# Optimization experiments

Hardware: AMD Instinct MI355X
Metric: run time of the kernel (lower is better)

Reference implementation:

```python
import jax, jax.numpy as jnp
import numpy as np

N_JOINTS = 24

def _rodrigues(r):
    # r: [B, J, 3] axis-angle -> [B, J, 3, 3] rotation matrices
    theta = jnp.clip(jnp.linalg.norm(r, axis=-1, keepdims=True), 1e-6)  # [B,J,1]
    rh = r / theta
    z = jnp.zeros_like(rh[..., :1])
    # skew-symmetric matrix m
    m = jnp.stack([
        jnp.concatenate([z, -rh[..., 2:3], rh[..., 1:2]], -1),
        jnp.concatenate([rh[..., 2:3], z, -rh[..., 0:1]], -1),
        jnp.concatenate([-rh[..., 1:2], rh[..., 0:1], z], -1),
    ], axis=-2)  # [B,J,3,3]
    rrT = rh[..., :, None] * rh[..., None, :]  # outer product [B,J,3,3]
    cos = jnp.cos(theta)[..., None]
    sin = jnp.sin(theta)[..., None]
    eye = jnp.eye(3, dtype=r.dtype)
    return cos * eye + (1.0 - cos) * rrT + sin * m

def _with_zeros(Rm, t):
    # Rm: [B,3,3], t: [B,3] -> [B,4,4] homogeneous transform
    B = Rm.shape[0]
    top = jnp.concatenate([Rm, t[:, :, None]], axis=-1)  # [B,3,4]
    bot = jnp.broadcast_to(jnp.array([0.0, 0.0, 0.0, 1.0], Rm.dtype), (B, 1, 4))
    return jnp.concatenate([top, bot], axis=1)

def _keypoints(v, idx):
    # v: [B,N,3], idx: [G,K] vertex-index groups -> [B,G,3] via (max+min)/2
    g = v[:, idx]  # [B,G,K,3] irregular gather
    return (g.max(axis=2) + g.min(axis=2)) * 0.5

def setup_inputs() -> dict:
    key = jax.random.key(0)
    ks = jax.random.split(key, 8)
    B, N, P, K = 64, 40000, 100, 128
    beta = jax.random.normal(ks[0], (B, P), jnp.float32)
    pose = jax.random.normal(ks[1], (B, N_JOINTS * 3), jnp.float32) * 0.3
    trans = jax.random.normal(ks[2], (B, 3), jnp.float32)
    shapedirs = jax.random.normal(ks[3], (P, 3 * N), jnp.float32) * 0.01
    v_template = jax.random.normal(ks[4], (N, 3), jnp.float32)
    w = jax.random.uniform(ks[5], (N, N_JOINTS), jnp.float32)
    weights = w / w.sum(axis=1, keepdims=True)  # LBS weights sum to 1
    reorder_index = jnp.arange(N_JOINTS, dtype=jnp.int64 if jax.config.jax_enable_x64 else jnp.int32)
    # kinematic tree: parent[i] < i (binary-tree shape stands in for the rabbit skeleton)
    parent = jnp.concatenate([jnp.zeros(1, jnp.int32), (jnp.arange(1, N_JOINTS, dtype=jnp.int32) - 1) // 2])
    joint_idx = jax.random.randint(ks[6], (N_JOINTS - 1, K), 0, N)
    add_idx = jax.random.randint(ks[7], (7, K), 0, N)
    return {"beta": beta, "pose": pose, "trans": trans, "shapedirs": shapedirs,
            "v_template": v_template, "weights": weights, "reorder_index": reorder_index,
            "parent": parent, "joint_idx": joint_idx, "add_idx": add_idx}

def reference(beta, pose, trans, shapedirs, v_template, weights,
              reorder_index, parent, joint_idx, add_idx):
    B = beta.shape[0]
    pose = pose.reshape(B, N_JOINTS, 3)[:, reorder_index]
    # blend shapes: v_shaped = beta @ shapedirs + template
    v_posed = (beta @ shapedirs + v_template.reshape(-1)).reshape(B, -1, 3)  # [B,N,3]
    # joints from vertex-group (max+min)/2, root is zero
    J = jnp.concatenate([jnp.zeros((B, 1, 3), beta.dtype), _keypoints(v_posed, joint_idx)], axis=1)  # [B,24,3]
    R = _rodrigues(pose)  # [B,24,3,3]
    # forward kinematics along the tree (fixed 24-joint loop)
    par = np.asarray(jax.device_get(parent))
    G = [_with_zeros(R[:, 0], J[:, 0])]
    for i in range(1, N_JOINTS):
        p = int(par[i])
        G_loc = _with_zeros(R[:, i], J[:, i] - J[:, p])
        G.append(jnp.matmul(G[p], G_loc))
    G = jnp.stack(G, axis=1)  # [B,24,4,4]
    # remove rest-pose joint locations (pack subtraction only touches last column)
    Jh = jnp.concatenate([J, jnp.zeros((B, N_JOINTS, 1), beta.dtype)], axis=-1)[..., None]  # [B,24,4,1]
    t_corr = jnp.matmul(G, Jh)  # [B,24,4,1]
    G1 = jnp.concatenate([G[..., :3], G[..., 3:4] - t_corr], axis=-1)
    # LBS skinning: per-vertex blended transform
    T = jnp.einsum('nk,bkij->bnij', weights, G1)  # [B,N,4,4]
    vh = jnp.concatenate([v_posed, jnp.ones((B, v_posed.shape[1], 1), beta.dtype)], axis=-1)  # [B,N,4]
    posed = jnp.einsum('bnij,bnj->bni', T, vh)[..., :3] + trans[:, None, :]  # [B,N,3]
    skeleton = jnp.concatenate([
        jnp.zeros((B, 1, 3), beta.dtype),
        _keypoints(posed, joint_idx),
        _keypoints(posed, add_idx),
    ], axis=1)  # [B,31,3]
    return posed, skeleton
```

## Files before the change

kernel.cpp:

```cpp
#include <hip/hip_runtime.h>
#include <math.h>

#define B   64
#define NV  40000
#define P   100
#define KG  128
#define NJ  24
#define TVJ 16
#define TVS 32
#define NSK 31
#define NSUB (KG / TVJ)

typedef __attribute__((ext_vector_type(8))) short bf16x8;
typedef __attribute__((ext_vector_type(4))) float f32x4;

__device__ __forceinline__ unsigned short rne_bf16(float f) {
  unsigned u = __float_as_uint(f);
  u = (u + 0x7FFFu + ((u >> 16) & 1u)) >> 16;
  return (unsigned short)u;
}

__global__ __launch_bounds__(512)
void k_jpart(const float* __restrict__ beta,
             const float* __restrict__ sd,
             const float* __restrict__ vt,
             const int*   __restrict__ joint_idx,
             float*       __restrict__ pmn,
             float*       __restrict__ pmx) {
  const int j = blockIdx.x;
  const int s = blockIdx.y;
  const int t = threadIdx.x;
  const int lane = t & 63, wv = t >> 6;
  const int l15 = lane & 15, qd = lane >> 4;

  __shared__ __align__(16) unsigned short beta_s[64 * 136];
  __shared__ __align__(16) unsigned short sdT_s[48 * 136];
  __shared__ float vt_s[48];
  __shared__ int   idx_s[TVJ];
  float* pos_s = (float*)beta_s;

  if (t < TVJ) idx_s[t] = joint_idx[j * KG + s * TVJ + t];
  __syncthreads();

  for (int e = t; e < 64 * 36; e += 512) {
    const int m = e / 36, pp = P + e % 36;
    beta_s[m * 136 + pp] = 0;
  }
  for (int e = t; e < 64 * P; e += 512) {
    const int m = e / P, p = e % P;
    beta_s[m * 136 + p] = rne_bf16(beta[e]);
  }
  for (int task = t; task < 768; task += 512) {
    const int n = task % 48, kg = task / 48;
    const size_t colbase = (size_t)idx_s[n / 3] * 3 + (n % 3);
    unsigned pk[4];
#pragma unroll
    for (int h = 0; h < 4; ++h) {
      const int k0 = kg * 8 + 2 * h;
      float f0 = 0.0f, f1 = 0.0f;
      if (k0 < P)     f0 = sd[(size_t)k0 * (3 * NV) + colbase];
      if (k0 + 1 < P) f1 = sd[(size_t)(k0 + 1) * (3 * NV) + colbase];
      pk[h] = (unsigned)rne_bf16(f0) | ((unsigned)rne_bf16(f1) << 16);
    }
    *(uint4*)&sdT_s[n * 136 + kg * 8] = make_uint4(pk[0], pk[1], pk[2], pk[3]);
  }
  if (t < 48) vt_s[t] = vt[(size_t)idx_s[t / 3] * 3 + (t % 3)];
  __syncthreads();

  f32x4 acc[3];
  float vtv[3];
  if (wv < 4) {
    bf16x8 af[4];
#pragma unroll
    for (int ks = 0; ks < 4; ++ks)
      af[ks] = *(const bf16x8*)&beta_s[(wv * 16 + l15) * 136 + ks * 32 + qd * 8];
#pragma unroll
    for (int nt = 0; nt < 3; ++nt) acc[nt] = (f32x4){0.f, 0.f, 0.f, 0.f};
#pragma unroll
    for (int ks = 0; ks < 4; ++ks) {
#pragma unroll
      for (int nt = 0; nt < 3; ++nt) {
        const bf16x8 bf = *(const bf16x8*)&sdT_s[(nt * 16 + l15) * 136 + ks * 32 + qd * 8];
        acc[nt] = __builtin_amdgcn_mfma_f32_16x16x32_bf16(af[ks], bf, acc[nt], 0, 0, 0);
      }
    }
#pragma unroll
    for (int nt = 0; nt < 3; ++nt) vtv[nt] = vt_s[nt * 16 + l15];
  }
  __syncthreads();

  if (wv < 4) {
#pragma unroll
    for (int nt = 0; nt < 3; ++nt) {
      const int n = nt * 16 + l15;
      const int v = n / 3, c = n - 3 * v;
#pragma unroll
      for (int r = 0; r < 4; ++r) {
        const int m = wv * 16 + qd * 4 + r;
        pos_s[m * 68 + v * 4 + c] = acc[nt][r] + vtv[nt];
      }
    }
  }
  __syncthreads();

  if (t < 192) {
    const int b = t / 3, c = t % 3;
    float lo = 1e30f, hi = -1e30f;
#pragma unroll
    for (int v = 0; v < TVJ; ++v) {
      const float val = pos_s[b * 68 + v * 4 + c];
      lo = fminf(lo, val); hi = fmaxf(hi, val);
    }
    pmn[((j * NSUB + s) * B + b) * 3 + c] = lo;
    pmx[((j * NSUB + s) * B + b) * 3 + c] = hi;
  }
}

__global__ void k_chain(const float* __restrict__ pose,
                        const int*   __restrict__ parent,
                        const float* __restrict__ pmn,
                        const float* __restrict__ pmx,
                        const float* __restrict__ beta,
                        const float* __restrict__ trans,
                        unsigned short* __restrict__ G1A,
                        unsigned short* __restrict__ beta_bf) {
  const int b = blockIdx.x;
  const int t = threadIdx.x;

  __shared__ float R[NJ][9];
  __shared__ float Jl[NJ][3];
  __shared__ float G[NJ][12];
  __shared__ float G1c[NJ][12];

  if (t < NJ) {
    const float x = pose[b * NJ * 3 + t * 3 + 0];
    const float y = pose[b * NJ * 3 + t * 3 + 1];
    const float z = pose[b * NJ * 3 + t * 3 + 2];
    const float th = fmaxf(sqrtf(x * x + y * y + z * z), 1e-6f);
    const float xh = x / th, yh = y / th, zh = z / th;
    const float c = cosf(th), s = sinf(th), o = 1.0f - c;
    R[t][0] = c + o * xh * xh;      R[t][1] = o * xh * yh - s * zh; R[t][2] = o * xh * zh + s * yh;
    R[t][3] = o * xh * yh + s * zh; R[t][4] = c + o * yh * yh;      R[t][5] = o * yh * zh - s * xh;
    R[t][6] = o * xh * zh - s * yh; R[t][7] = o * yh * zh + s * xh; R[t][8] = c + o * zh * zh;
    if (t == 0) {
      Jl[0][0] = 0.0f; Jl[0][1] = 0.0f; Jl[0][2] = 0.0f;
    } else {
      const int jj = t - 1;
#pragma unroll
      for (int c2 = 0; c2 < 3; ++c2) {
        float lo = 1e30f, hi = -1e30f;
#pragma unroll
        for (int s2 = 0; s2 < NSUB; ++s2) {
          lo = fminf(lo, pmn[((jj * NSUB + s2) * B + b) * 3 + c2]);
          hi = fmaxf(hi, pmx[((jj * NSUB + s2) * B + b) * 3 + c2]);
        }
        Jl[t][c2] = 0.5f * (lo + hi);
      }
    }
  }
  __syncthreads();

  if (t < 12) {
    const int r = t >> 2, c = t & 3;
    G[0][t] = (c < 3) ? R[0][r * 3 + c] : Jl[0][r];
  }
  __syncthreads();

  for (int i = 1; i < NJ; ++i) {
    const int p = parent[i];
    if (t < 12) {
      const int r = t >> 2, c = t & 3;
      const float g0 = G[p][r * 4 + 0];
      const float g1 = G[p][r * 4 + 1];
      const float g2 = G[p][r * 4 + 2];
      float l0, l1, l2, add;
      if (c < 3) {
        l0 = R[i][0 * 3 + c]; l1 = R[i][1 * 3 + c]; l2 = R[i][2 * 3 + c];
        add = 0.0f;
      } else {
        l0 = Jl[i][0] - Jl[p][0]; l1 = Jl[i][1] - Jl[p][1]; l2 = Jl[i][2] - Jl[p][2];
        add = G[p][r * 4 + 3];
      }
      G[i][t] = g0 * l0 + g1 * l1 + g2 * l2 + add;
    }
    __syncthreads();
  }

  for (int e = t; e < NJ * 12; e += 64) {
    const int i = e / 12, rc = e % 12, r = rc >> 2, c = rc & 3;
    float val;
    if (c < 3) {
      val = G[i][rc];
    } else {
      val = G[i][r * 4 + 3] - (G[i][r * 4 + 0] * Jl[i][0] +
                               G[i][r * 4 + 1] * Jl[i][1] +
                               G[i][r * 4 + 2] * Jl[i][2]);
    }
    G1c[i][rc] = val;
  }
  __syncthreads();

  for (int e = t; e < 136; e += 64)
    beta_bf[b * 136 + e] = (e < P) ? rne_bf16(beta[b * P + e]) : (unsigned short)0;

  for (int e = t; e < 512; e += 64) {
    const int m = e >> 5, k = e & 31;
    float val = 0.0f;
    if (m < 12) {
      if (k < NJ) val = G1c[k][m];
      else if (k == NJ && (m & 3) == 3) val = trans[b * 3 + (m >> 2)];
    }
    G1A[(size_t)b * 512 + e] = rne_bf16(val);
  }
}

__global__ __launch_bounds__(256)
void k_skin(const float* __restrict__ sd,
            const float* __restrict__ vt,
            const float* __restrict__ w,
            const unsigned short* __restrict__ beta_bf,
            const unsigned short* __restrict__ G1A,
            float*       __restrict__ out) {
  const int n0v  = blockIdx.x * TVS;
  const int col0 = n0v * 3;
  const int t  = threadIdx.x;
  const int lane = t & 63, wv = t >> 6;
  const int l15 = lane & 15, q = lane >> 4;

  __shared__ __align__(16) unsigned char smem[46464];
  unsigned short* beta_s = (unsigned short*)smem;
  unsigned short* sdT_s  = (unsigned short*)(smem + 17408);
  unsigned short* wT_s   = (unsigned short*)(smem + 43520);
  float*          vt_s   = (float*)(smem + 46080);
  float*          vhf    = (float*)smem;

  for (int e = t; e < 1088; e += 256)
    ((uint4*)beta_s)[e] = ((const uint4*)beta_bf)[e];
  for (int task = t; task < 1536; task += 256) {
    const int n = task % 96, kg = task / 96;
    unsigned pk[4];
#pragma unroll
    for (int h = 0; h < 4; ++h) {
      const int k0 = kg * 8 + 2 * h;
      float f0 = 0.0f, f1 = 0.0f;
      if (k0 < P)     f0 = sd[(size_t)k0 * (3 * NV) + col0 + n];
      if (k0 + 1 < P) f1 = sd[(size_t)(k0 + 1) * (3 * NV) + col0 + n];
      pk[h] = (unsigned)rne_bf16(f0) | ((unsigned)rne_bf16(f1) << 16);
    }
    *(uint4*)&sdT_s[n * 136 + kg * 8] = make_uint4(pk[0], pk[1], pk[2], pk[3]);
  }
  for (int e = t; e < 1024; e += 256) {
    const int n = e >> 5, k = e & 31;
    float val = (k < NJ) ? w[(n0v + n) * NJ + k] : (k == NJ ? 1.0f : 0.0f);
    wT_s[n * 40 + k] = rne_bf16(val);
  }
  if (t < 96) vt_s[t] = vt[col0 + t];
  __syncthreads();

  bf16x8 af[4];
#pragma unroll
  for (int ks = 0; ks < 4; ++ks)
    af[ks] = *(const bf16x8*)&beta_s[(wv * 16 + l15) * 136 + ks * 32 + q * 8];
  f32x4 acc[6];
#pragma unroll
  for (int nt = 0; nt < 6; ++nt) acc[nt] = (f32x4){0.f, 0.f, 0.f, 0.f};
#pragma unroll
  for (int ks = 0; ks < 4; ++ks) {
#pragma unroll
    for (int nt = 0; nt < 6; ++nt) {
      const bf16x8 bf = *(const bf16x8*)&sdT_s[(nt * 16 + l15) * 136 + ks * 32 + q * 8];
      acc[nt] = __builtin_amdgcn_mfma_f32_16x16x32_bf16(af[ks], bf, acc[nt], 0, 0, 0);
    }
  }
  __syncthreads();

#pragma unroll
  for (int nt = 0; nt < 6; ++nt) {
    const int n = nt * 16 + l15;
    const int v = n / 3, c = n - 3 * v;
    const float vtn = vt_s[n];
#pragma unroll
    for (int r = 0; r < 4; ++r) {
      const int m = wv * 16 + q * 4 + r;
      vhf[m * 128 + v * 4 + c] = acc[nt][r] + vtn;
    }
  }
  __syncthreads();

  const bf16x8 wf0 = *(const bf16x8*)&wT_s[l15 * 40 + q * 8];
  const bf16x8 wf1 = *(const bf16x8*)&wT_s[(16 + l15) * 40 + q * 8];
  const f32x4 zero = (f32x4){0.f, 0.f, 0.f, 0.f};
#pragma unroll 4
  for (int bi = 0; bi < 16; ++bi) {
    const int b = wv * 16 + bi;
    const bf16x8 gf = *(const bf16x8*)&G1A[(size_t)b * 512 + l15 * 32 + q * 8];
    const f32x4 d0 = __builtin_amdgcn_mfma_f32_16x16x32_bf16(gf, wf0, zero, 0, 0, 0);
    const f32x4 d1 = __builtin_amdgcn_mfma_f32_16x16x32_bf16(gf, wf1, zero, 0, 0, 0);
    const float4 vh0 = *(const float4*)&vhf[b * 128 + l15 * 4];
    const float4 vh1 = *(const float4*)&vhf[b * 128 + 64 + l15 * 4];
    if (q < 3) {
      out[(size_t)b * (NV * 3) + col0 + l15 * 3 + q] =
          d0[0] * vh0.x + d0[1] * vh0.y + d0[2] * vh0.z + d0[3];
      out[(size_t)b * (NV * 3) + col0 + 48 + l15 * 3 + q] =
          d1[0] * vh1.x + d1[1] * vh1.y + d1[2] * vh1.z + d1[3];
    }
  }
}

__global__ void k_skel(const float* __restrict__ posed,
                       const int*   __restrict__ joint_idx,
                       const int*   __restrict__ add_idx,
                       float*       __restrict__ skel) {
  const int j = blockIdx.x;
  const int b = blockIdx.y;
  const int t = threadIdx.x;
  const int idx = (j < 23) ? joint_idx[j * KG + t] : add_idx[(j - 23) * KG + t];

  const float* p = posed + (size_t)b * NV * 3 + (size_t)idx * 3;
  float mn[3], mx[3];
#pragma unroll
  for (int c = 0; c < 3; ++c) { mn[c] = p[c]; mx[c] = p[c]; }
#pragma unroll
  for (int off = 32; off > 0; off >>= 1) {
#pragma unroll
    for (int c = 0; c < 3; ++c) {
      mn[c] = fminf(mn[c], __shfl_down(mn[c], off));
      mx[c] = fmaxf(mx[c], __shfl_down(mx[c], off));
    }
  }
  __shared__ float s_mn[2][3], s_mx[2][3];
  const int wave = t >> 6, lane = t & 63;
  if (lane == 0) {
#pragma unroll
    for (int c = 0; c < 3; ++c) { s_mn[wave][c] = mn[c]; s_mx[wave][c] = mx[c]; }
  }
  __syncthreads();
  if (t == 0) {
#pragma unroll
    for (int c = 0; c < 3; ++c) {
      float lo = fminf(s_mn[0][c], s_mn[1][c]);
      float hi = fmaxf(s_mx[0][c], s_mx[1][c]);
      skel[(b * NSK + 1 + j) * 3 + c] = 0.5f * (lo + hi);
      if (j == 0) skel[(b * NSK + 0) * 3 + c] = 0.0f;
    }
  }
}

extern "C" void kernel_launch(void* const* d_in, const int* in_sizes, int n_in,
                              void* d_out, int out_size, void* d_ws, size_t ws_size,
                              hipStream_t stream) {
  const float* beta     = (const float*)d_in[0];
  const float* pose     = (const float*)d_in[1];
  const float* trans    = (const float*)d_in[2];
  const float* sd       = (const float*)d_in[3];
  const float* vt       = (const float*)d_in[4];
  const float* w        = (const float*)d_in[5];
  const int* parent     = (const int*)d_in[7];
  const int* joint_idx  = (const int*)d_in[8];
  const int* add_idx    = (const int*)d_in[9];

  float* out = (float*)d_out;
  unsigned short* G1A     = (unsigned short*)d_ws;
  unsigned short* beta_bf = G1A + B * 512;
  float* pmn = (float*)(beta_bf + B * 136);
  float* pmx = pmn + 23 * NSUB * B * 3;

  k_jpart<<<dim3(23, NSUB), 512, 0, stream>>>(beta, sd, vt, joint_idx, pmn, pmx);
  k_chain<<<B, 64, 0, stream>>>(pose, parent, pmn, pmx, beta, trans, G1A, beta_bf);
  k_skin <<<NV / TVS, 256, 0, stream>>>(sd, vt, w, beta_bf, G1A, out);
  k_skel <<<dim3(30, B), 128, 0, stream>>>(out, joint_idx, add_idx,
                                           out + (size_t)B * NV * 3);
}
```

Before: 160.2 us.

## Fuse four kernels into two using atomic last-block and spin-wait tails

Merges the joint-partial kernel with the kinematic chain, so the last block to finish (found with an atomic counter) computes the forward kinematics for all 64 batches, one thread per batch. The skinning and skeleton kernels are also merged. The final 160 skinning blocks spin on a global counter until every block has written its output, then each does a share of the keypoint min/max reductions. This cuts launch count and inter-kernel gaps. The cost is a serial tail on one block, spin-waiting that depends on the waiting blocks being co-resident, and an extra memset launch.

```diff
diff --git a/kernel.cpp b/kernel.cpp
--- a/kernel.cpp
+++ b/kernel.cpp
@@ -1,15 +1,18 @@
 #include <hip/hip_runtime.h>
 #include <math.h>
 
-#define B   64
-#define NV  40000
-#define P   100
-#define KG  128
-#define NJ  24
-#define TVJ 16
-#define TVS 32
-#define NSK 31
+#define B    64
+#define NV   40000
+#define P    100
+#define KG   128
+#define NJ   24
+#define TVJ  16
+#define TVS  32
+#define NSK  31
 #define NSUB (KG / TVJ)
+#define NBLK (NV / TVS)
+#define NSPIN 160
+#define NTASK (30 * B)
 
 typedef __attribute__((ext_vector_type(8))) short bf16x8;
 typedef __attribute__((ext_vector_type(4))) float f32x4;
@@ -20,37 +23,44 @@
   return (unsigned short)u;
 }
 
-__global__ __launch_bounds__(512)
-void k_jpart(const float* __restrict__ beta,
-             const float* __restrict__ sd,
-             const float* __restrict__ vt,
-             const int*   __restrict__ joint_idx,
-             float*       __restrict__ pmn,
-             float*       __restrict__ pmx) {
+__global__ __launch_bounds__(256)
+void k_jc(const float* __restrict__ beta,
+          const float* __restrict__ sd,
+          const float* __restrict__ vt,
+          const int*   __restrict__ joint_idx,
+          const float* __restrict__ pose,
+          const float* __restrict__ trans,
+          float*       __restrict__ pmn,
+          float*       __restrict__ pmx,
+          unsigned short* __restrict__ G1A,
+          unsigned short* __restrict__ beta_bf,
+          int*         __restrict__ cnt) {
   const int j = blockIdx.x;
   const int s = blockIdx.y;
   const int t = threadIdx.x;
   const int lane = t & 63, wv = t >> 6;
   const int l15 = lane & 15, qd = lane >> 4;
 
-  __shared__ __align__(16) unsigned short beta_s[64 * 136];
-  __shared__ __align__(16) unsigned short sdT_s[48 * 136];
-  __shared__ float vt_s[48];
-  __shared__ int   idx_s[TVJ];
-  float* pos_s = (float*)beta_s;
+  __shared__ __align__(16) unsigned char smem[55296];
+  unsigned short* beta_s = (unsigned short*)smem;
+  unsigned short* sdT_s  = (unsigned short*)(smem + 17408);
+  float*          vt_s   = (float*)(smem + 30464);
+  int*            idx_s  = (int*)(smem + 30656);
+  float*          pos_s  = (float*)smem;
+  __shared__ int s_old;
 
   if (t < TVJ) idx_s[t] = joint_idx[j * KG + s * TVJ + t];
   __syncthreads();
 
-  for (int e = t; e < 64 * 36; e += 512) {
+  for (int e = t; e < 64 * 36; e += 256) {
     const int m = e / 36, pp = P + e % 36;
     beta_s[m * 136 + pp] = 0;
   }
-  for (int e = t; e < 64 * P; e += 512) {
+  for (int e = t; e < 64 * P; e += 256) {
     const int m = e / P, p = e % P;
     beta_s[m * 136 + p] = rne_bf16(beta[e]);
   }
-  for (int task = t; task < 768; task += 512) {
+  for (int task = t; task < 768; task += 256) {
     const int n = task % 48, kg = task / 48;
     const size_t colbase = (size_t)idx_s[n / 3] * 3 + (n % 3);
     unsigned pk[4];
@@ -67,38 +77,34 @@
   if (t < 48) vt_s[t] = vt[(size_t)idx_s[t / 3] * 3 + (t % 3)];
   __syncthreads();
 
+  bf16x8 af[4];
+#pragma unroll
+  for (int ks = 0; ks < 4; ++ks)
+    af[ks] = *(const bf16x8*)&beta_s[(wv * 16 + l15) * 136 + ks * 32 + qd * 8];
   f32x4 acc[3];
+#pragma unroll
+  for (int nt = 0; nt < 3; ++nt) acc[nt] = (f32x4){0.f, 0.f, 0.f, 0.f};
+#pragma unroll
+  for (int ks = 0; ks < 4; ++ks) {
+#pragma unroll
+    for (int nt = 0; nt < 3; ++nt) {
+      const bf16x8 bf = *(const bf16x8*)&sdT_s[(nt * 16 + l15) * 136 + ks * 32 + qd * 8];
+      acc[nt] = __builtin_amdgcn_mfma_f32_16x16x32_bf16(af[ks], bf, acc[nt], 0, 0, 0);
+    }
+  }
   float vtv[3];
-  if (wv < 4) {
-    bf16x8 af[4];
-#pragma unroll
-    for (int ks = 0; ks < 4; ++ks)
-      af[ks] = *(const bf16x8*)&beta_s[(wv * 16 + l15) * 136 + ks * 32 + qd * 8];
-#pragma unroll
-    for (int nt = 0; nt < 3; ++nt) acc[nt] = (f32x4){0.f, 0.f, 0.f, 0.f};
-#pragma unroll
-    for (int ks = 0; ks < 4; ++ks) {
-#pragma unroll
-      for (int nt = 0; nt < 3; ++nt) {
-        const bf16x8 bf = *(const bf16x8*)&sdT_s[(nt * 16 + l15) * 136 + ks * 32 + qd * 8];
-        acc[nt] = __builtin_amdgcn_mfma_f32_16x16x32_bf16(af[ks], bf, acc[nt], 0, 0, 0);
-      }
-    }
-#pragma unroll
-    for (int nt = 0; nt < 3; ++nt) vtv[nt] = vt_s[nt * 16 + l15];
-  }
-  __syncthreads();
-
-  if (wv < 4) {
-#pragma unroll
-    for (int nt = 0; nt < 3; ++nt) {
-      const int n = nt * 16 + l15;
-      const int v = n / 3, c = n - 3 * v;
-#pragma unroll
-      for (int r = 0; r < 4; ++r) {
-        const int m = wv * 16 + qd * 4 + r;
-        pos_s[m * 68 + v * 4 + c] = acc[nt][r] + vtv[nt];
-      }
+#pragma unroll
+  for (int nt = 0; nt < 3; ++nt) vtv[nt] = vt_s[nt * 16 + l15];
+  __syncthreads();
+
+#pragma unroll
+  for (int nt = 0; nt < 3; ++nt) {
+    const int n = nt * 16 + l15;
+    const int v = n / 3, c = n - 3 * v;
+#pragma unroll
+    for (int r = 0; r < 4; ++r) {
+      const int m = wv * 16 + qd * 4 + r;
+      pos_s[m * 68 + v * 4 + c] = acc[nt][r] + vtv[nt];
     }
   }
   __syncthreads();
@@ -114,113 +120,125 @@
     pmn[((j * NSUB + s) * B + b) * 3 + c] = lo;
     pmx[((j * NSUB + s) * B + b) * 3 + c] = hi;
   }
+
+  __syncthreads();
+  if (t == 0) { __threadfence(); s_old = atomicAdd(cnt, 1); }
+  __syncthreads();
+  if (s_old != 23 * NSUB - 1) return;
+  __threadfence();
+
+  float* Jl_c = (float*)smem;
+  float* Gl   = (float*)(smem + 18432);
+
+  {
+    const uint4 z4 = make_uint4(0, 0, 0, 0);
+    for (int e = t; e < 4096; e += 256) ((uint4*)G1A)[e] = z4;
+  }
+  for (int e = t; e < 64 * 136; e += 256) {
+    const int b = e / 136, k = e - b * 136;
+    beta_bf[e] = (k < P) ? rne_bf16(beta[b * P + k]) : (unsigned short)0;
+  }
+  for (int e = t; e < 192; e += 256) Jl_c[e] = 0.0f;
+  for (int e = t; e < 23 * 192; e += 256) {
+    const int jj = e / 192, rem = e - jj * 192;
+    const int b = rem / 3, c = rem - b * 3;
+    float lo = 1e30f, hi = -1e30f;
+#pragma unroll
+    for (int s2 = 0; s2 < NSUB; ++s2) {
+      lo = fminf(lo, pmn[(jj * NSUB + s2) * 192 + rem]);
+      hi = fmaxf(hi, pmx[(jj * NSUB + s2) * 192 + rem]);
+    }
+    Jl_c[((jj + 1) * 3 + c) * 64 + b] = 0.5f * (lo + hi);
+  }
+  __syncthreads();
+
+  if (t < 64) {
+    const int b = t;
+    float px = pose[b * 72 + 0], py = pose[b * 72 + 1], pz = pose[b * 72 + 2];
+    float G_[12];
+#pragma unroll 1
+    for (int i = 0; i < NJ; ++i) {
+      float nx = 0.f, ny = 0.f, nz = 0.f;
+      if (i < NJ - 1) {
+        nx = pose[b * 72 + (i + 1) * 3 + 0];
+        ny = pose[b * 72 + (i + 1) * 3 + 1];
+        nz = pose[b * 72 + (i + 1) * 3 + 2];
+      }
+      const float th = fmaxf(sqrtf(px * px + py * py + pz * pz), 1e-6f);
+      const float xh = px / th, yh = py / th, zh = pz / th;
+      const float cc = cosf(th), ss = sinf(th), oo = 1.0f - cc;
+      float R9[9];
+      R9[0] = cc + oo * xh * xh;      R9[1] = oo * xh * yh - ss * zh; R9[2] = oo * xh * zh + ss * yh;
+      R9[3] = oo * xh * yh + ss * zh; R9[4] = cc + oo * yh * yh;      R9[5] = oo * yh * zh - ss * xh;
+      R9[6] = oo * xh * zh - ss * yh; R9[7] = oo * yh * zh + ss * xh; R9[8] = cc + oo * zh * zh;
+
+      const float ji0 = Jl_c[(i * 3 + 0) * 64 + b];
+      const float ji1 = Jl_c[(i * 3 + 1) * 64 + b];
+      const float ji2 = Jl_c[(i * 3 + 2) * 64 + b];
+
+      if (i == 0) {
+#pragma unroll
+        for (int r = 0; r < 3; ++r) {
+          G_[r * 4 + 0] = R9[r * 3 + 0];
+          G_[r * 4 + 1] = R9[r * 3 + 1];
+          G_[r * 4 + 2] = R9[r * 3 + 2];
+          G_[r * 4 + 3] = 0.0f;
+        }
+      } else {
+        const int p = (i - 1) >> 1;
+        const float d0 = ji0 - Jl_c[(p * 3 + 0) * 64 + b];
+        const float d1 = ji1 - Jl_c[(p * 3 + 1) * 64 + b];
+        const float d2 = ji2 - Jl_c[(p * 3 + 2) * 64 + b];
+        float Gn[12];
+#pragma unroll
+        for (int r = 0; r < 3; ++r) {
+          const float g0 = Gl[(b * 12 + p) * 12 + r * 4 + 0];
+          const float g1 = Gl[(b * 12 + p) * 12 + r * 4 + 1];
+          const float g2 = Gl[(b * 12 + p) * 12 + r * 4 + 2];
+          const float g3 = Gl[(b * 12 + p) * 12 + r * 4 + 3];
+          Gn[r * 4 + 0] = g0 * R9[0] + g1 * R9[3] + g2 * R9[6];
+          Gn[r * 4 + 1] = g0 * R9[1] + g1 * R9[4] + g2 * R9[7];
+          Gn[r * 4 + 2] = g0 * R9[2] + g1 * R9[5] + g2 * R9[8];
+          Gn[r * 4 + 3] = g0 * d0 + g1 * d1 + g2 * d2 + g3;
+        }
+#pragma unroll
+        for (int e = 0; e < 12; ++e) G_[e] = Gn[e];
+      }
+      if (i < 12) {
+#pragma unroll
+        for (int e = 0; e < 12; ++e) Gl[(b * 12 + i) * 12 + e] = G_[e];
+      }
+#pragma unroll
+      for (int r = 0; r < 3; ++r) {
+        const float tc = G_[r * 4 + 0] * ji0 + G_[r * 4 + 1] * ji1 + G_[r * 4 + 2] * ji2;
+        G1A[b * 512 + (r * 4 + 0) * 32 + i] = rne_bf16(G_[r * 4 + 0]);
+        G1A[b * 512 + (r * 4 + 1) * 32 + i] = rne_bf16(G_[r * 4 + 1]);
+        G1A[b * 512 + (r * 4 + 2) * 32 + i] = rne_bf16(G_[r * 4 + 2]);
+        G1A[b * 512 + (r * 4 + 3) * 32 + i] = rne_bf16(G_[r * 4 + 3] - tc);
+      }
+      px = nx; py = ny; pz = nz;
+    }
+  } else if (t >= 192) {
+#pragma unroll
+    for (int k = 0; k < 3; ++k) {
+      const int e = (t - 192) * 3 + k;
+      const int b = e / 3, r = e - b * 3;
+      G1A[b * 512 + (r * 4 + 3) * 32 + 24] = rne_bf16(trans[b * 3 + r]);
+    }
+  }
 }
 
-__global__ void k_chain(const float* __restrict__ pose,
-                        const int*   __restrict__ parent,
-                        const float* __restrict__ pmn,
-                        const float* __restrict__ pmx,
-                        const float* __restrict__ beta,
-                        const float* __restrict__ trans,
-                        unsigned short* __restrict__ G1A,
-                        unsigned short* __restrict__ beta_bf) {
-  const int b = blockIdx.x;
-  const int t = threadIdx.x;
-
-  __shared__ float R[NJ][9];
-  __shared__ float Jl[NJ][3];
-  __shared__ float G[NJ][12];
-  __shared__ float G1c[NJ][12];
-
-  if (t < NJ) {
-    const float x = pose[b * NJ * 3 + t * 3 + 0];
-    const float y = pose[b * NJ * 3 + t * 3 + 1];
-    const float z = pose[b * NJ * 3 + t * 3 + 2];
-    const float th = fmaxf(sqrtf(x * x + y * y + z * z), 1e-6f);
-    const float xh = x / th, yh = y / th, zh = z / th;
-    const float c = cosf(th), s = sinf(th), o = 1.0f - c;
-    R[t][0] = c + o * xh * xh;      R[t][1] = o * xh * yh - s * zh; R[t][2] = o * xh * zh + s * yh;
-    R[t][3] = o * xh * yh + s * zh; R[t][4] = c + o * yh * yh;      R[t][5] = o * yh * zh - s * xh;
-    R[t][6] = o * xh * zh - s * yh; R[t][7] = o * yh * zh + s * xh; R[t][8] = c + o * zh * zh;
-    if (t == 0) {
-      Jl[0][0] = 0.0f; Jl[0][1] = 0.0f; Jl[0][2] = 0.0f;
-    } else {
-      const int jj = t - 1;
-#pragma unroll
-      for (int c2 = 0; c2 < 3; ++c2) {
-        float lo = 1e30f, hi = -1e30f;
-#pragma unroll
-        for (int s2 = 0; s2 < NSUB; ++s2) {
-          lo = fminf(lo, pmn[((jj * NSUB + s2) * B + b) * 3 + c2]);
-          hi = fmaxf(hi, pmx[((jj * NSUB + s2) * B + b) * 3 + c2]);
-        }
-        Jl[t][c2] = 0.5f * (lo + hi);
-      }
-    }
-  }
-  __syncthreads();
-
-  if (t < 12) {
-    const int r = t >> 2, c = t & 3;
-    G[0][t] = (c < 3) ? R[0][r * 3 + c] : Jl[0][r];
-  }
-  __syncthreads();
-
-  for (int i = 1; i < NJ; ++i) {
-    const int p = parent[i];
-    if (t < 12) {
-      const int r = t >> 2, c = t & 3;
-      const float g0 = G[p][r * 4 + 0];
-      const float g1 = G[p][r * 4 + 1];
-      const float g2 = G[p][r * 4 + 2];
-      float l0, l1, l2, add;
-      if (c < 3) {
-        l0 = R[i][0 * 3 + c]; l1 = R[i][1 * 3 + c]; l2 = R[i][2 * 3 + c];
-        add = 0.0f;
-      } else {
-        l0 = Jl[i][0] - Jl[p][0]; l1 = Jl[i][1] - Jl[p][1]; l2 = Jl[i][2] - Jl[p][2];
-        add = G[p][r * 4 + 3];
-      }
-      G[i][t] = g0 * l0 + g1 * l1 + g2 * l2 + add;
-    }
-    __syncthreads();
-  }
-
-  for (int e = t; e < NJ * 12; e += 64) {
-    const int i = e / 12, rc = e % 12, r = rc >> 2, c = rc & 3;
-    float val;
-    if (c < 3) {
-      val = G[i][rc];
-    } else {
-      val = G[i][r * 4 + 3] - (G[i][r * 4 + 0] * Jl[i][0] +
-                               G[i][r * 4 + 1] * Jl[i][1] +
-                               G[i][r * 4 + 2] * Jl[i][2]);
-    }
-    G1c[i][rc] = val;
-  }
-  __syncthreads();
-
-  for (int e = t; e < 136; e += 64)
-    beta_bf[b * 136 + e] = (e < P) ? rne_bf16(beta[b * P + e]) : (unsigned short)0;
-
-  for (int e = t; e < 512; e += 64) {
-    const int m = e >> 5, k = e & 31;
-    float val = 0.0f;
-    if (m < 12) {
-      if (k < NJ) val = G1c[k][m];
-      else if (k == NJ && (m & 3) == 3) val = trans[b * 3 + (m >> 2)];
-    }
-    G1A[(size_t)b * 512 + e] = rne_bf16(val);
-  }
-}
-
 __global__ __launch_bounds__(256)
-void k_skin(const float* __restrict__ sd,
-            const float* __restrict__ vt,
-            const float* __restrict__ w,
-            const unsigned short* __restrict__ beta_bf,
-            const unsigned short* __restrict__ G1A,
-            float*       __restrict__ out) {
+void k_ss(const float* __restrict__ sd,
+          const float* __restrict__ vt,
+          const float* __restrict__ w,
+          const unsigned short* __restrict__ beta_bf,
+          const unsigned short* __restrict__ G1A,
+          const int*   __restrict__ joint_idx,
+          const int*   __restrict__ add_idx,
+          float*       __restrict__ out,
+          float*       __restrict__ skel,
+          int*         __restrict__ cnt) {
   const int n0v  = blockIdx.x * TVS;
   const int col0 = n0v * 3;
   const int t  = threadIdx.x;
@@ -233,6 +251,7 @@
   unsigned short* wT_s   = (unsigned short*)(smem + 43520);
   float*          vt_s   = (float*)(smem + 46080);
   float*          vhf    = (float*)smem;
+  __shared__ int s_old;
 
   for (int e = t; e < 1088; e += 256)
     ((uint4*)beta_s)[e] = ((const uint4*)beta_bf)[e];
@@ -305,44 +324,60 @@
           d1[0] * vh1.x + d1[1] * vh1.y + d1[2] * vh1.z + d1[3];
     }
   }
-}
-
-__global__ void k_skel(const float* __restrict__ posed,
-                       const int*   __restrict__ joint_idx,
-                       const int*   __restrict__ add_idx,
-                       float*       __restrict__ skel) {
-  const int j = blockIdx.x;
-  const int b = blockIdx.y;
-  const int t = threadIdx.x;
-  const int idx = (j < 23) ? joint_idx[j * KG + t] : add_idx[(j - 23) * KG + t];
-
-  const float* p = posed + (size_t)b * NV * 3 + (size_t)idx * 3;
-  float mn[3], mx[3];
-#pragma unroll
-  for (int c = 0; c < 3; ++c) { mn[c] = p[c]; mx[c] = p[c]; }
-#pragma unroll
-  for (int off = 32; off > 0; off >>= 1) {
-#pragma unroll
-    for (int c = 0; c < 3; ++c) {
-      mn[c] = fminf(mn[c], __shfl_down(mn[c], off));
-      mx[c] = fmaxf(mx[c], __shfl_down(mx[c], off));
-    }
-  }
-  __shared__ float s_mn[2][3], s_mx[2][3];
-  const int wave = t >> 6, lane = t & 63;
-  if (lane == 0) {
-#pragma unroll
-    for (int c = 0; c < 3; ++c) { s_mn[wave][c] = mn[c]; s_mx[wave][c] = mx[c]; }
-  }
-  __syncthreads();
+
+  __syncthreads();
+  if (t == 0) { __threadfence(); s_old = atomicAdd(cnt, 1); }
+  __syncthreads();
+  const int old = s_old;
+  if (old < NBLK - NSPIN) return;
   if (t == 0) {
-#pragma unroll
-    for (int c = 0; c < 3; ++c) {
-      float lo = fminf(s_mn[0][c], s_mn[1][c]);
-      float hi = fmaxf(s_mx[0][c], s_mx[1][c]);
-      skel[(b * NSK + 1 + j) * 3 + c] = 0.5f * (lo + hi);
-      if (j == 0) skel[(b * NSK + 0) * 3 + c] = 0.0f;
-    }
+    while (__hip_atomic_load(cnt, __ATOMIC_RELAXED, __HIP_MEMORY_SCOPE_AGENT) < NBLK)
+      __builtin_amdgcn_s_sleep(2);
+  }
+  __syncthreads();
+  __threadfence();
+  const int rank = old - (NBLK - NSPIN);
+
+  float* s_red = (float*)smem;
+  const int h  = t >> 7;
+  const int th = t & 127;
+  const int wvh = th >> 6, ln = th & 63;
+#pragma unroll 1
+  for (int rd = 0; rd < 6; ++rd) {
+    const int task = rank * 12 + rd * 2 + h;
+    const int jj = task >> 6;
+    const int b  = task & 63;
+    const int idx = (jj < 23) ? joint_idx[jj * KG + th] : add_idx[(jj - 23) * KG + th];
+    const float* pp = out + (size_t)b * NV * 3 + (size_t)idx * 3;
+    float mn[3], mx[3];
+#pragma unroll
+    for (int c = 0; c < 3; ++c) { mn[c] = pp[c]; mx[c] = pp[c]; }
+#pragma unroll
+    for (int off = 32; off > 0; off >>= 1) {
+#pragma unroll
+      for (int c = 0; c < 3; ++c) {
+        mn[c] = fminf(mn[c], __shfl_down(mn[c], off));
+        mx[c] = fmaxf(mx[c], __shfl_down(mx[c], off));
+      }
+    }
+    if (ln == 0) {
+#pragma unroll
+      for (int c = 0; c < 3; ++c) {
+        s_red[(h * 2 + wvh) * 6 + c]     = mn[c];
+        s_red[(h * 2 + wvh) * 6 + 3 + c] = mx[c];
+      }
+    }
+    __syncthreads();
+    if (th == 0) {
+#pragma unroll
+      for (int c = 0; c < 3; ++c) {
+        const float lo = fminf(s_red[(h * 2) * 6 + c],     s_red[(h * 2 + 1) * 6 + c]);
+        const float hi = fmaxf(s_red[(h * 2) * 6 + 3 + c], s_red[(h * 2 + 1) * 6 + 3 + c]);
+        skel[(b * NSK + 1 + jj) * 3 + c] = 0.5f * (lo + hi);
+        if (jj == 0) skel[(b * NSK + 0) * 3 + c] = 0.0f;
+      }
+    }
+    __syncthreads();
   }
 }
 
@@ -355,19 +390,20 @@
   const float* sd       = (const float*)d_in[3];
   const float* vt       = (const float*)d_in[4];
   const float* w        = (const float*)d_in[5];
-  const int* parent     = (const int*)d_in[7];
   const int* joint_idx  = (const int*)d_in[8];
   const int* add_idx    = (const int*)d_in[9];
 
-  float* out = (float*)d_out;
+  float* out  = (float*)d_out;
+  float* skel = out + (size_t)B * NV * 3;
   unsigned short* G1A     = (unsigned short*)d_ws;
   unsigned short* beta_bf = G1A + B * 512;
   float* pmn = (float*)(beta_bf + B * 136);
   float* pmx = pmn + 23 * NSUB * B * 3;
-
-  k_jpart<<<dim3(23, NSUB), 512, 0, stream>>>(beta, sd, vt, joint_idx, pmn, pmx);
-  k_chain<<<B, 64, 0, stream>>>(pose, parent, pmn, pmx, beta, trans, G1A, beta_bf);
-  k_skin <<<NV / TVS, 256, 0, stream>>>(sd, vt, w, beta_bf, G1A, out);
-  k_skel <<<dim3(30, B), 128, 0, stream>>>(out, joint_idx, add_idx,
-                                           out + (size_t)B * NV * 3);
+  int*   cnt = (int*)(pmx + 23 * NSUB * B * 3);
+
+  hipMemsetAsync(cnt, 0, 16, stream);
+  k_jc<<<dim3(23, NSUB), 256, 0, stream>>>(beta, sd, vt, joint_idx, pose, trans,
+                                           pmn, pmx, G1A, beta_bf, cnt + 0);
+  k_ss<<<NBLK, 256, 0, stream>>>(sd, vt, w, beta_bf, G1A, joint_idx, add_idx,
+                                 out, skel, cnt + 1);
 }
```

Result: slower. 248.0 us (+54.8%).
